# Performance work log

Measured on AMD Instinct MI355X. Metric: run time of the kernel, lower is better.

## Reference

```python
import jax, jax.numpy as jnp
import numpy as np

B, N, C = 32, 197, 768   # batch, tokens (num_patches+1), emb_dim
KW = 197                 # kw_dim = seq_len
L = 12                   # num_layers (weights shared, norms per-layer)
HID = 3072               # mlp hidden = 4*emb_dim


def layer_norm(x, g, b, eps=1e-5):
    mu = jnp.mean(x, axis=-1, keepdims=True)
    var = jnp.var(x, axis=-1, keepdims=True)
    return (x - mu) * jax.lax.rsqrt(var + eps) * g + b


def attention(x, qkv_w, fc_w, fc_b, ln_g, ln_b, fc2_w, fc2_b, num_heads):
    b, n, c = x.shape
    d = c // num_heads
    qkv = (x @ qkv_w).reshape(b, n, 3, num_heads, d)
    q = qkv[:, :, 0].transpose(0, 2, 1, 3)  # [B,H,N,d]
    k = qkv[:, :, 1].transpose(0, 2, 1, 3)
    v = qkv[:, :, 2].transpose(0, 2, 1, 3)
    scale = d ** -0.5
    attn = jnp.einsum('bhnd,bhmd->bhnm', q, k) * scale      # [B,H,N,N]
    attn = attn @ fc_w + fc_b                                # [B,H,N,KW]
    attn = layer_norm(attn, ln_g, ln_b)
    attn = jax.nn.softmax(attn, axis=-1)
    attn = attn.transpose(0, 1, 3, 2)                        # [B,H,KW,N]
    y = jnp.einsum('bhkn,bhnd->bhkd', attn, v)               # [B,H,KW,d]
    # fc2 applied along KW axis of y.transpose(-2,-1): out[b,h,n,d]
    out = jnp.einsum('bhkd,kn->bnhd', y, fc2_w) + fc2_b[None, :, None, None]
    return out.reshape(b, n, c)


def mlp(x, w1, b1, w2, b2):
    return jax.nn.gelu(x @ w1 + b1, approximate=False) @ w2 + b2


def setup_inputs() -> dict:
    key = jax.random.key(0)
    ks = jax.random.split(key, 16)
    s = 0.02
    return {
        'x': jax.random.normal(ks[0], (B, N, C), jnp.float32),
        'qkv_w': jax.random.normal(ks[1], (C, 3 * C), jnp.float32) * s,
        'fc_w': jax.random.normal(ks[2], (N, KW), jnp.float32) * s,
        'fc_b': jnp.zeros((KW,), jnp.float32),
        'attn_ln_g': jnp.ones((KW,), jnp.float32),
        'attn_ln_b': jnp.zeros((KW,), jnp.float32),
        'fc2_w': jax.random.normal(ks[3], (KW, N), jnp.float32) * s,
        'fc2_b': jnp.zeros((N,), jnp.float32),
        'mlp_w1': jax.random.normal(ks[4], (C, HID), jnp.float32) * s,
        'mlp_b1': jnp.zeros((HID,), jnp.float32),
        'mlp_w2': jax.random.normal(ks[5], (HID, C), jnp.float32) * s,
        'mlp_b2': jnp.zeros((C,), jnp.float32),
        'f_ln_g': jnp.ones((L, C), jnp.float32),
        'f_ln_b': jnp.zeros((L, C), jnp.float32),
        'g_ln_g': jnp.ones((L, C), jnp.float32),
        'g_ln_b': jnp.zeros((L, C), jnp.float32),
        'num_heads': 12,
    }


def reference(x, qkv_w, fc_w, fc_b, attn_ln_g, attn_ln_b, fc2_w, fc2_b,
              mlp_w1, mlp_b1, mlp_w2, mlp_b2, f_ln_g, f_ln_b, g_ln_g, g_ln_b,
              num_heads):
    # x -> cat([x,x]) -> reversible stack -> mean of the two halves
    x1, x2 = x, x
    n_layers = f_ln_g.shape[0]
    for i in range(n_layers):
        # y1 = x1 + f(x2); y2 = x2 + g(y1)  (PreNorm wraps f and g)
        y1 = x1 + attention(layer_norm(x2, f_ln_g[i], f_ln_b[i]),
                            qkv_w, fc_w, fc_b, attn_ln_g, attn_ln_b,
                            fc2_w, fc2_b, num_heads)
        y2 = x2 + mlp(layer_norm(y1, g_ln_g[i], g_ln_b[i]),
                      mlp_w1, mlp_b1, mlp_w2, mlp_b2)
        x1, x2 = y1, y2
    return (x1 + x2) * 0.5
```

## Files before the change

kernel.cpp:

```cpp
#include <hip/hip_runtime.h>
#include <math.h>

#define BB   32
#define NN   197
#define CC   768
#define HH   12
#define DD   64
#define KWW  197
#define HIDD 3072
#define NL   12
#define RR   (BB*NN)
#define BHH  (BB*HH)
#define NP   224

typedef __attribute__((ext_vector_type(8))) short short8;
typedef __attribute__((ext_vector_type(4))) float floatx4;
typedef __attribute__((ext_vector_type(4))) unsigned short us4;

__device__ __forceinline__ unsigned short f2bf(float f) {
    unsigned int u = __float_as_uint(f);
    u += 0x7fff + ((u >> 16) & 1);
    return (unsigned short)(u >> 16);
}

__global__ void ln768_kernel(const float* __restrict__ in, const float* __restrict__ g,
                             const float* __restrict__ be, unsigned short* __restrict__ out) {
    int row = blockIdx.x;
    const float* x = in + (size_t)row * CC;
    unsigned short* o = out + (size_t)row * CC;
    int t = threadIdx.x;
    float v0 = x[t], v1 = x[t+256], v2 = x[t+512];
    float s = v0+v1+v2;
    float q = v0*v0+v1*v1+v2*v2;
    for (int off = 1; off < 64; off <<= 1) {
        s += __shfl_xor(s, off, 64);
        q += __shfl_xor(q, off, 64);
    }
    __shared__ float sh[8];
    int wv = t >> 6, ln = t & 63;
    if (ln == 0) { sh[wv] = s; sh[4+wv] = q; }
    __syncthreads();
    s = sh[0]+sh[1]+sh[2]+sh[3];
    q = sh[4]+sh[5]+sh[6]+sh[7];
    float mu  = s * (1.0f/CC);
    float var = q * (1.0f/CC) - mu*mu;
    float rs  = rsqrtf(var + 1e-5f);
    o[t]     = f2bf((v0-mu)*rs*g[t]     + be[t]);
    o[t+256] = f2bf((v1-mu)*rs*g[t+256] + be[t+256]);
    o[t+512] = f2bf((v2-mu)*rs*g[t+512] + be[t+512]);
}

__global__ void init_ln(const float* __restrict__ x, float* __restrict__ x1,
                        float* __restrict__ x2,
                        const float* __restrict__ g, const float* __restrict__ be,
                        unsigned short* __restrict__ out) {
    int row = blockIdx.x;
    const float* xp = x + (size_t)row * CC;
    int t = threadIdx.x;
    float v0 = xp[t], v1 = xp[t+256], v2 = xp[t+512];
    float* a = x1 + (size_t)row * CC;
    float* b = x2 + (size_t)row * CC;
    a[t] = v0; a[t+256] = v1; a[t+512] = v2;
    b[t] = v0; b[t+256] = v1; b[t+512] = v2;
    float s = v0+v1+v2;
    float q = v0*v0+v1*v1+v2*v2;
    for (int off = 1; off < 64; off <<= 1) {
        s += __shfl_xor(s, off, 64);
        q += __shfl_xor(q, off, 64);
    }
    __shared__ float sh[8];
    int wv = t >> 6, ln = t & 63;
    if (ln == 0) { sh[wv] = s; sh[4+wv] = q; }
    __syncthreads();
    s = sh[0]+sh[1]+sh[2]+sh[3];
    q = sh[4]+sh[5]+sh[6]+sh[7];
    float mu  = s * (1.0f/CC);
    float var = q * (1.0f/CC) - mu*mu;
    float rs  = rsqrtf(var + 1e-5f);
    unsigned short* o = out + (size_t)row * CC;
    o[t]     = f2bf((v0-mu)*rs*g[t]     + be[t]);
    o[t+256] = f2bf((v1-mu)*rs*g[t+256] + be[t+256]);
    o[t+512] = f2bf((v2-mu)*rs*g[t+512] + be[t+512]);
}

__global__ void reduce_ln(float* __restrict__ x2, const float* __restrict__ part,
                          const float* __restrict__ b2,
                          const float* __restrict__ g, const float* __restrict__ be,
                          unsigned short* __restrict__ out,
                          const float* __restrict__ x1f, float* __restrict__ outf,
                          int mode) {
    int row = blockIdx.x;
    float* xp = x2 + (size_t)row * CC;
    const float* p0 = part + (size_t)row * CC;
    const float* p1 = part + (size_t)RR*CC + (size_t)row * CC;
    int t = threadIdx.x;
    float v0 = xp[t]     + p0[t]     + p1[t]     + b2[t];
    float v1 = xp[t+256] + p0[t+256] + p1[t+256] + b2[t+256];
    float v2 = xp[t+512] + p0[t+512] + p1[t+512] + b2[t+512];
    xp[t] = v0; xp[t+256] = v1; xp[t+512] = v2;
    if (mode == 2) {
        const float* xo = x1f + (size_t)row * CC;
        float* o = outf + (size_t)row * CC;
        o[t]     = 0.5f*(xo[t]     + v0);
        o[t+256] = 0.5f*(xo[t+256] + v1);
        o[t+512] = 0.5f*(xo[t+512] + v2);
        return;
    }
    float s = v0+v1+v2;
    float q = v0*v0+v1*v1+v2*v2;
    for (int off = 1; off < 64; off <<= 1) {
        s += __shfl_xor(s, off, 64);
        q += __shfl_xor(q, off, 64);
    }
    __shared__ float sh[8];
    int wv = t >> 6, ln = t & 63;
    if (ln == 0) { sh[wv] = s; sh[4+wv] = q; }
    __syncthreads();
    s = sh[0]+sh[1]+sh[2]+sh[3];
    q = sh[4]+sh[5]+sh[6]+sh[7];
    float mu  = s * (1.0f/CC);
    float var = q * (1.0f/CC) - mu*mu;
    float rs  = rsqrtf(var + 1e-5f);
    unsigned short* o = out + (size_t)row * CC;
    o[t]     = f2bf((v0-mu)*rs*g[t]     + be[t]);
    o[t+256] = f2bf((v1-mu)*rs*g[t+256] + be[t+256]);
    o[t+512] = f2bf((v2-mu)*rs*g[t+512] + be[t+512]);
}

__global__ void transpose_cast(const float* __restrict__ in, unsigned short* __restrict__ out,
                               int K, int Nd, int Kpad) {
    __shared__ float tile[32][33];
    int n0 = blockIdx.x*32, k0 = blockIdx.y*32;
    int tx = threadIdx.x & 31, ty = threadIdx.x >> 5;
    #pragma unroll
    for (int i = 0; i < 4; i++) {
        int k = k0 + ty + i*8;
        tile[ty + i*8][tx] = (k < K && n0+tx < Nd) ? in[(size_t)k*Nd + n0 + tx] : 0.f;
    }
    __syncthreads();
    #pragma unroll
    for (int i = 0; i < 4; i++) {
        int n = n0 + ty + i*8;
        if (n < Nd && k0 + tx < Kpad) out[(size_t)n*Kpad + k0 + tx] = f2bf(tile[tx][ty + i*8]);
    }
}

template<int EPI, int KS>
__global__ __launch_bounds__(256) void gemm128(
    const unsigned short* __restrict__ A, const unsigned short* __restrict__ Bt,
    const float* __restrict__ bias, float* __restrict__ Cf, unsigned short* __restrict__ Cb,
    int M, int Nd, int K)
{
    __shared__ unsigned short As[2*128*64];
    __shared__ unsigned short Bs[2*128*64];
    int tid  = threadIdx.x;
    int wv   = tid >> 6, lane = tid & 63;
    int wm   = wv >> 1, wn = wv & 1;
    int quad = lane >> 4, mrow = lane & 15;
    int rl   = lane >> 3, ps = lane & 7;

    int gx   = gridDim.x;
    int nwg  = gx * gridDim.y;
    int orig = blockIdx.y * gx + blockIdx.x;
    int qq = nwg >> 3, rr = nwg & 7;
    int xcd = orig & 7, idx = orig >> 3;
    int wg  = (xcd < rr ? xcd*(qq+1) : rr*(qq+1) + (xcd-rr)*qq) + idx;
    int bm  = (wg / gx) * 128;
    int bn  = (wg % gx) * 128;

    const int Kc    = K / KS;
    const int kbase = (KS > 1) ? blockIdx.z * Kc : 0;
    const int nt    = Kc / 64;

    floatx4 acc[4][4];
    #pragma unroll
    for (int i = 0; i < 4; i++)
        #pragma unroll
        for (int j = 0; j < 4; j++) acc[i][j] = (floatx4){0.f,0.f,0.f,0.f};

#define G128_STAGE(buf, kcol)                                                     \
    do {                                                                          \
        _Pragma("unroll")                                                         \
        for (int i_ = 0; i_ < 4; i_++) {                                          \
            int r_ = wv*32 + i_*8 + rl;                                           \
            int sl_ = ps ^ (r_ & 7);                                              \
            int gr_ = bm + r_; if (gr_ > M-1) gr_ = M-1;                          \
            __builtin_amdgcn_global_load_lds(                                     \
                (const __attribute__((address_space(1))) void*)(A + (size_t)gr_*K + (kcol) + sl_*8), \
                (__attribute__((address_space(3))) void*)(As + (buf)*8192 + (wv*32 + i_*8)*64), \
                16, 0, 0);                                                        \
        }                                                                         \
        _Pragma("unroll")                                                         \
        for (int i_ = 0; i_ < 4; i_++) {                                          \
            int r_ = wv*32 + i_*8 + rl;                                           \
            int sl_ = ps ^ (r_ & 7);                                              \
            int gr_ = bn + r_;                                                    \
            __builtin_amdgcn_global_load_lds(                                     \
                (const __attribute__((address_space(1))) void*)(Bt + (size_t)gr_*K + (kcol) + sl_*8), \
                (__attribute__((address_space(3))) void*)(Bs + (buf)*8192 + (wv*32 + i_*8)*64), \
                16, 0, 0);                                                        \
        }                                                                         \
    } while (0)

    G128_STAGE(0, kbase);
    __syncthreads();

    for (int t = 0; t < nt; ++t) {
        const int c = t & 1;
        if (t + 1 < nt) G128_STAGE(c ^ 1, kbase + (t+1)*64);
        const int cb = c * 8192;
        #pragma unroll
        for (int kk = 0; kk < 2; kk++) {
            short8 af[4], bf[4];
            #pragma unroll
            for (int mi = 0; mi < 4; mi++) {
                int lr = wm*64 + mi*16 + mrow;
                af[mi] = *(const short8*)&As[cb + lr*64 + (((kk<<2)|quad) ^ (lr & 7))*8];
            }
            #pragma unroll
            for (int ni = 0; ni < 4; ni++) {
                int lr = wn*64 + ni*16 + mrow;
                bf[ni] = *(const short8*)&Bs[cb + lr*64 + (((kk<<2)|quad) ^ (lr & 7))*8];
            }
            #pragma unroll
            for (int mi = 0; mi < 4; mi++)
                #pragma unroll
                for (int ni = 0; ni < 4; ni++)
                    acc[mi][ni] = __builtin_amdgcn_mfma_f32_16x16x32_bf16(
                        af[mi], bf[ni], acc[mi][ni], 0, 0, 0);
        }
        __syncthreads();
    }
#undef G128_STAGE

    float* Cfz = (EPI == 5) ? (Cf + (size_t)blockIdx.z * M * Nd) : Cf;
    #pragma unroll
    for (int mi = 0; mi < 4; mi++) {
        int row0 = bm + wm*64 + mi*16 + quad*4;
        #pragma unroll
        for (int ni = 0; ni < 4; ni++) {
            int col = bn + wn*64 + ni*16 + mrow;
            float bv = (EPI == 2) ? bias[col] : 0.f;
            #pragma unroll
            for (int r = 0; r < 4; r++) {
                int row = row0 + r;
                if (row >= M) continue;
                float v = acc[mi][ni][r] + bv;
                if (EPI == 2) {
                    v = v / (1.0f + __expf(-1.5957691216f*v*(1.0f + 0.044715f*v*v)));
                    Cb[(size_t)row*Nd + col] = f2bf(v);
                } else if (EPI == 5) {
                    Cfz[(size_t)row*Nd + col] = v;
                } else if (EPI == 4) {
                    int sel = col / CC;
                    int rem = col - sel*CC;
                    int h = rem >> 6, d = rem & 63;
                    int b = row / NN, n = row - b*NN;
                    int bh = b*HH + h;
                    unsigned short val = f2bf(v);
                    if (sel < 2)
                        Cb[((size_t)sel*BHH + bh)*NN*DD + (size_t)n*DD + d] = val;
                    else
                        Cb[(size_t)2*BHH*NN*DD + (size_t)bh*DD*NP + (size_t)d*NP + n] = val;
                }
            }
        }
    }
}

__global__ __launch_bounds__(256) void attn_score(
    const unsigned short* __restrict__ qb,
    const unsigned short* __restrict__ kb,
    const unsigned short* __restrict__ fw,
    const float* __restrict__ fbias,
    const float* __restrict__ g, const float* __restrict__ be,
    unsigned short* __restrict__ PT)
{
    int bh = blockIdx.y;
    int bm = blockIdx.x * 64;
    __shared__ unsigned short Ks[224*DD];
    __shared__ unsigned short S1s[64*NP];
    __shared__ unsigned short Bs[224*32];
    __shared__ float gls[NP], bls[NP], bbs[NP];
    int tid = threadIdx.x;
    if (tid < NP) {
        bool vc = tid < KWW;
        gls[tid] = vc ? g[tid]     : 1.f;
        bls[tid] = vc ? be[tid]    : 0.f;
        bbs[tid] = vc ? fbias[tid] : 0.f;
    }
    int wv = tid >> 6, lane = tid & 63;
    int quad = lane >> 4, mrow = lane & 15;

    {
        int lrow = lane >> 3, lko = (lane & 7) * 8;
        #pragma unroll
        for (int i = 0; i < 7; i++) {
            int r = wv*56 + i*8 + lrow;
            __builtin_amdgcn_global_load_lds(
                (const __attribute__((address_space(1))) void*)(kb + ((size_t)bh*NN + r)*DD + lko),
                (__attribute__((address_space(3))) void*)(Ks + (size_t)(wv*56 + i*8)*DD),
                16, 0, 0);
        }
    }
    int qrow = bm + wv*16 + mrow; if (qrow > NN-1) qrow = NN-1;
    short8 aq0 = *(const short8*)&qb[((size_t)bh*NN + qrow)*DD + quad*8];
    short8 aq1 = *(const short8*)&qb[((size_t)bh*NN + qrow)*DD + 32 + quad*8];
    __syncthreads();

    #pragma unroll
    for (int ni = 0; ni < 14; ni++) {
        floatx4 a = (floatx4){0.f,0.f,0.f,0.f};
        short8 bf0 = *(const short8*)&Ks[(size_t)(ni*16 + mrow)*DD + quad*8];
        short8 bf1 = *(const short8*)&Ks[(size_t)(ni*16 + mrow)*DD + 32 + quad*8];
        a = __builtin_amdgcn_mfma_f32_16x16x32_bf16(aq0, bf0, a, 0, 0, 0);
        a = __builtin_amdgcn_mfma_f32_16x16x32_bf16(aq1, bf1, a, 0, 0, 0);
        #pragma unroll
        for (int r = 0; r < 4; r++)
            S1s[(size_t)(wv*16 + quad*4 + r)*NP + ni*16 + mrow] = f2bf(a[r]*0.125f);
    }
    __syncthreads();

    floatx4 acc[14];
    #pragma unroll
    for (int j = 0; j < 14; j++) acc[j] = (floatx4){0.f,0.f,0.f,0.f};
    for (int k0 = 0; k0 < 7; k0++) {
        for (int c = wv; c < 14; c += 4) {
            int gr = c*16 + (lane >> 2); if (gr > KWW-1) gr = KWW-1;
            __builtin_amdgcn_global_load_lds(
                (const __attribute__((address_space(1))) void*)(fw + (size_t)gr*NP + k0*32 + (lane & 3)*8),
                (__attribute__((address_space(3))) void*)(Bs + (size_t)(c*16)*32),
                16, 0, 0);
        }
        __syncthreads();
        short8 af = *(const short8*)&S1s[(size_t)(wv*16 + mrow)*NP + k0*32 + quad*8];
        #pragma unroll
        for (int ni = 0; ni < 14; ni++) {
            short8 bf = *(const short8*)&Bs[(size_t)(ni*16 + mrow)*32 + quad*8];
            acc[ni] = __builtin_amdgcn_mfma_f32_16x16x32_bf16(af, bf, acc[ni], 0, 0, 0);
        }
        __syncthreads();
    }

    float s[4] = {}, q[4] = {};
    #pragma unroll
    for (int ni = 0; ni < 14; ni++) {
        int col = ni*16 + mrow;
        float cm = (col < KWW) ? 1.f : 0.f;
        #pragma unroll
        for (int r = 0; r < 4; r++) {
            float x = acc[ni][r] + bbs[col];
            acc[ni][r] = x;
            s[r] += x*cm; q[r] += x*x*cm;
        }
    }
    #pragma unroll
    for (int o = 1; o < 16; o <<= 1)
        #pragma unroll
        for (int r = 0; r < 4; r++) {
            s[r] += __shfl_xor(s[r], o, 64);
            q[r] += __shfl_xor(q[r], o, 64);
        }
    float mu[4], rs[4], mx[4];
    #pragma unroll
    for (int r = 0; r < 4; r++) {
        mu[r] = s[r] * (1.0f/KWW);
        float var = q[r] * (1.0f/KWW) - mu[r]*mu[r];
        rs[r] = rsqrtf(var + 1e-5f);
        mx[r] = -1e30f;
    }
    #pragma unroll
    for (int ni = 0; ni < 14; ni++) {
        int col = ni*16 + mrow;
        bool vc = col < KWW;
        #pragma unroll
        for (int r = 0; r < 4; r++) {
            float x = (acc[ni][r] - mu[r]) * rs[r] * gls[col] + bls[col];
            acc[ni][r] = x;
            if (vc) mx[r] = fmaxf(mx[r], x);
        }
    }
    #pragma unroll
    for (int o = 1; o < 16; o <<= 1)
        #pragma unroll
        for (int r = 0; r < 4; r++)
            mx[r] = fmaxf(mx[r], __shfl_xor(mx[r], o, 64));
    float se[4] = {};
    #pragma unroll
    for (int ni = 0; ni < 14; ni++) {
        int col = ni*16 + mrow;
        float cm = (col < KWW) ? 1.f : 0.f;
        #pragma unroll
        for (int r = 0; r < 4; r++) {
            float p = __expf(acc[ni][r] - mx[r]) * cm;
            acc[ni][r] = p;
            se[r] += p;
        }
    }
    #pragma unroll
    for (int o = 1; o < 16; o <<= 1)
        #pragma unroll
        for (int r = 0; r < 4; r++)
            se[r] += __shfl_xor(se[r], o, 64);
    unsigned short* Pb = PT + (size_t)bh*NP*NP;
    int row0 = bm + wv*16 + quad*4;
    float inv0 = 1.0f/se[0], inv1 = 1.0f/se[1], inv2 = 1.0f/se[2], inv3 = 1.0f/se[3];
    #pragma unroll
    for (int ni = 0; ni < 14; ni++) {
        int col = ni*16 + mrow;
        if (col >= KWW) continue;
        if (row0 + 3 < NN) {
            us4 o = { f2bf(acc[ni][0]*inv0), f2bf(acc[ni][1]*inv1),
                      f2bf(acc[ni][2]*inv2), f2bf(acc[ni][3]*inv3) };
            *(us4*)&Pb[(size_t)col*NP + row0] = o;
        } else {
            float invs[4] = {inv0, inv1, inv2, inv3};
            #pragma unroll
            for (int r = 0; r < 4; r++)
                if (row0 + r < NN)
                    Pb[(size_t)col*NP + row0 + r] = f2bf(acc[ni][r]*invs[r]);
        }
    }
}

__global__ __launch_bounds__(256) void attn_out2(
    const unsigned short* __restrict__ PT,
    const unsigned short* __restrict__ vT,
    const unsigned short* __restrict__ fw,
    const float* __restrict__ bias,
    float* __restrict__ x1)
{
    int dt = blockIdx.x;
    int bh = blockIdx.y; int b = bh / HH, h = bh - b*HH;
    __shared__ unsigned short yT[16*232];
    int wv = threadIdx.x >> 6, lane = threadIdx.x & 63;
    int quad = lane >> 4, mrow = lane & 15;
    const unsigned short* Pb = PT + (size_t)bh*NP*NP;
    const unsigned short* Vb = vT + (size_t)bh*DD*NP + (size_t)(dt*16)*NP;

    short8 bfv[7];
    #pragma unroll
    for (int kc = 0; kc < 7; kc++)
        bfv[kc] = *(const short8*)&Vb[(size_t)mrow*NP + kc*32 + quad*8];
    #pragma unroll
    for (int i = 0; i < 2; i++) {
        int t0 = wv + i*8, t1 = t0 + 4;
        bool v1 = t1 < 14;
        floatx4 a0 = (floatx4){0.f,0.f,0.f,0.f};
        floatx4 a1 = (floatx4){0.f,0.f,0.f,0.f};
        #pragma unroll
        for (int kc = 0; kc < 7; kc++) {
            short8 p0 = *(const short8*)&Pb[(size_t)(t0*16 + mrow)*NP + kc*32 + quad*8];
            a0 = __builtin_amdgcn_mfma_f32_16x16x32_bf16(p0, bfv[kc], a0, 0, 0, 0);
            if (v1) {
                short8 p1 = *(const short8*)&Pb[(size_t)(t1*16 + mrow)*NP + kc*32 + quad*8];
                a1 = __builtin_amdgcn_mfma_f32_16x16x32_bf16(p1, bfv[kc], a1, 0, 0, 0);
            }
        }
        us4 o0 = { f2bf(a0[0]), f2bf(a0[1]), f2bf(a0[2]), f2bf(a0[3]) };
        *(us4*)&yT[mrow*232 + t0*16 + quad*4] = o0;
        if (v1) {
            us4 o1 = { f2bf(a1[0]), f2bf(a1[1]), f2bf(a1[2]), f2bf(a1[3]) };
            *(us4*)&yT[mrow*232 + t1*16 + quad*4] = o1;
        }
    }
    __syncthreads();

    short8 yf[7];
    #pragma unroll
    for (int kc = 0; kc < 7; kc++)
        yf[kc] = *(const short8*)&yT[mrow*232 + kc*32 + quad*8];
    float* xb = x1 + (size_t)b*NN*CC + (size_t)h*DD + dt*16 + mrow;
    #pragma unroll
    for (int i = 0; i < 2; i++) {
        int n0t = wv + i*8, n1t = n0t + 4;
        bool v1 = n1t < 13;
        floatx4 a0 = (floatx4){0.f,0.f,0.f,0.f};
        floatx4 a1 = (floatx4){0.f,0.f,0.f,0.f};
        #pragma unroll
        for (int kc = 0; kc < 7; kc++) {
            short8 f0 = *(const short8*)&fw[(size_t)(n0t*16 + mrow)*NP + kc*32 + quad*8];
            a0 = __builtin_amdgcn_mfma_f32_16x16x32_bf16(f0, yf[kc], a0, 0, 0, 0);
            if (v1) {
                short8 f1 = *(const short8*)&fw[(size_t)(n1t*16 + mrow)*NP + kc*32 + quad*8];
                a1 = __builtin_amdgcn_mfma_f32_16x16x32_bf16(f1, yf[kc], a1, 0, 0, 0);
            }
        }
        #pragma unroll
        for (int r = 0; r < 4; r++) {
            int n = n0t*16 + quad*4 + r;
            if (n < NN) xb[(size_t)n*CC] += a0[r] + bias[n];
        }
        if (v1) {
            #pragma unroll
            for (int r = 0; r < 4; r++) {
                int n = n1t*16 + quad*4 + r;
                if (n < NN) xb[(size_t)n*CC] += a1[r] + bias[n];
            }
        }
    }
}

extern "C" void kernel_launch(void* const* d_in, const int* in_sizes, int n_in,
                              void* d_out, int out_size, void* d_ws, size_t ws_size,
                              hipStream_t stream) {
    const float* x     = (const float*)d_in[0];
    const float* qkv_w = (const float*)d_in[1];
    const float* fc_w  = (const float*)d_in[2];
    const float* fc_b  = (const float*)d_in[3];
    const float* alng  = (const float*)d_in[4];
    const float* alnb  = (const float*)d_in[5];
    const float* fc2w  = (const float*)d_in[6];
    const float* fc2b  = (const float*)d_in[7];
    const float* w1    = (const float*)d_in[8];
    const float* b1    = (const float*)d_in[9];
    const float* w2    = (const float*)d_in[10];
    const float* b2    = (const float*)d_in[11];
    const float* flng  = (const float*)d_in[12];
    const float* flnb  = (const float*)d_in[13];
    const float* glng  = (const float*)d_in[14];
    const float* glnb  = (const float*)d_in[15];
    float* out = (float*)d_out;

    float* ws = (float*)d_ws;
    size_t off = 0;
    float* x1 = ws + off; off += (size_t)RR*CC;
    float* x2 = ws + off; off += (size_t)RR*CC;
    float* part = ws + off; off += (size_t)2*RR*CC;
    unsigned short* lnb = (unsigned short*)(ws + off); off += (size_t)RR*CC/2;
    unsigned short* qkvo = (unsigned short*)(ws + off);
    unsigned short* qb = qkvo;
    unsigned short* kb = qkvo + (size_t)BHH*NN*DD;
    unsigned short* vT = qkvo + (size_t)2*BHH*NN*DD;
    off += ((size_t)2*BHH*NN*DD + (size_t)BHH*DD*NP + 1) / 2;
    unsigned short* PT   = (unsigned short*)(ws + off); off += (size_t)BHH*NP*NP/2;
    unsigned short* hid  = (unsigned short*)(ws + off); off += (size_t)RR*HIDD/2;
    unsigned short* qkv_wt = (unsigned short*)(ws + off); off += (size_t)3*CC*CC/2;
    unsigned short* w1t    = (unsigned short*)(ws + off); off += (size_t)CC*HIDD/2;
    unsigned short* w2t    = (unsigned short*)(ws + off); off += (size_t)CC*HIDD/2;
    unsigned short* fc_wt  = (unsigned short*)(ws + off); off += (size_t)NN*NP/2 + 16;
    unsigned short* fc2_wt = (unsigned short*)(ws + off); off += (size_t)NP*NP/2 + 16;

    hipMemsetAsync(vT, 0, (size_t)BHH*DD*NP*2, stream);
    hipMemsetAsync(fc2_wt, 0, (size_t)NP*NP*2, stream);

    transpose_cast<<<dim3(72, 24), 256, 0, stream>>>(qkv_w, qkv_wt, CC, 3*CC, CC);
    transpose_cast<<<dim3(96, 24), 256, 0, stream>>>(w1, w1t, CC, HIDD, CC);
    transpose_cast<<<dim3(24, 96), 256, 0, stream>>>(w2, w2t, HIDD, CC, HIDD);
    transpose_cast<<<dim3(7, 7),   256, 0, stream>>>(fc_w,  fc_wt,  NN, KWW, NP);
    transpose_cast<<<dim3(7, 7),   256, 0, stream>>>(fc2w,  fc2_wt, KWW, NN, NP);

    init_ln<<<RR, 256, 0, stream>>>(x, x1, x2, flng, flnb, lnb);

    const int MT = (RR + 127) / 128;
    for (int l = 0; l < NL; l++) {
        gemm128<4,1><<<dim3(3*CC/128, MT), 256, 0, stream>>>(
            lnb, qkv_wt, nullptr, nullptr, qb, RR, 3*CC, CC);
        attn_score<<<dim3(4, BHH), 256, 0, stream>>>(
            qb, kb, fc_wt, fc_b, alng, alnb, PT);
        attn_out2<<<dim3(4, BHH), 256, 0, stream>>>(PT, vT, fc2_wt, fc2b, x1);
        ln768_kernel<<<RR, 256, 0, stream>>>(x1, glng + l*CC, glnb + l*CC, lnb);
        gemm128<2,1><<<dim3(HIDD/128, MT), 256, 0, stream>>>(
            lnb, w1t, b1, nullptr, hid, RR, HIDD, CC);
        gemm128<5,2><<<dim3(CC/128, MT, 2), 256, 0, stream>>>(
            hid, w2t, nullptr, part, nullptr, RR, CC, HIDD);
        if (l + 1 < NL) {
            reduce_ln<<<RR, 256, 0, stream>>>(
                x2, part, b2, flng + (l+1)*CC, flnb + (l+1)*CC, lnb,
                nullptr, nullptr, 1);
        } else {
            reduce_ln<<<RR, 256, 0, stream>>>(
                x2, part, b2, nullptr, nullptr, nullptr, x1, out, 2);
        }
    }
}
```

Before: 3.624 ms.

## Single-buffer GEMM LDS tiles and read fc weights directly from global in attn_score

The main GEMM drops its double-buffered LDS prefetch and now loads each K tile, syncs, and computes, which halves its shared memory and may allow more resident blocks, at the cost of losing load/compute overlap. In attn_score the fc weight tile is no longer staged through LDS with two barriers per K step. Each lane now reads its B fragments straight from global memory, and the A fragments are preloaded into registers. The S1 row stride is padded to 232 to reduce bank conflicts, and the fc weight buffer is zero-padded to 224 rows so the direct reads stay in bounds.

```diff
diff --git a/kernel.cpp b/kernel.cpp
--- a/kernel.cpp
+++ b/kernel.cpp
@@ -12,6 +12,7 @@
 #define RR   (BB*NN)
 #define BHH  (BB*HH)
 #define NP   224
+#define SLS  232
 
 typedef __attribute__((ext_vector_type(8))) short short8;
 typedef __attribute__((ext_vector_type(4))) float floatx4;
@@ -151,8 +152,8 @@
     const float* __restrict__ bias, float* __restrict__ Cf, unsigned short* __restrict__ Cb,
     int M, int Nd, int K)
 {
-    __shared__ unsigned short As[2*128*64];
-    __shared__ unsigned short Bs[2*128*64];
+    __shared__ unsigned short As[128*64];
+    __shared__ unsigned short Bs[128*64];
     int tid  = threadIdx.x;
     int wv   = tid >> 6, lane = tid & 63;
     int wm   = wv >> 1, wn = wv & 1;
@@ -170,7 +171,6 @@
 
     const int Kc    = K / KS;
     const int kbase = (KS > 1) ? blockIdx.z * Kc : 0;
-    const int nt    = Kc / 64;
 
     floatx4 acc[4][4];
     #pragma unroll
@@ -178,49 +178,40 @@
         #pragma unroll
         for (int j = 0; j < 4; j++) acc[i][j] = (floatx4){0.f,0.f,0.f,0.f};
 
-#define G128_STAGE(buf, kcol)                                                     \
-    do {                                                                          \
-        _Pragma("unroll")                                                         \
-        for (int i_ = 0; i_ < 4; i_++) {                                          \
-            int r_ = wv*32 + i_*8 + rl;                                           \
-            int sl_ = ps ^ (r_ & 7);                                              \
-            int gr_ = bm + r_; if (gr_ > M-1) gr_ = M-1;                          \
-            __builtin_amdgcn_global_load_lds(                                     \
-                (const __attribute__((address_space(1))) void*)(A + (size_t)gr_*K + (kcol) + sl_*8), \
-                (__attribute__((address_space(3))) void*)(As + (buf)*8192 + (wv*32 + i_*8)*64), \
-                16, 0, 0);                                                        \
-        }                                                                         \
-        _Pragma("unroll")                                                         \
-        for (int i_ = 0; i_ < 4; i_++) {                                          \
-            int r_ = wv*32 + i_*8 + rl;                                           \
-            int sl_ = ps ^ (r_ & 7);                                              \
-            int gr_ = bn + r_;                                                    \
-            __builtin_amdgcn_global_load_lds(                                     \
-                (const __attribute__((address_space(1))) void*)(Bt + (size_t)gr_*K + (kcol) + sl_*8), \
-                (__attribute__((address_space(3))) void*)(Bs + (buf)*8192 + (wv*32 + i_*8)*64), \
-                16, 0, 0);                                                        \
-        }                                                                         \
-    } while (0)
-
-    G128_STAGE(0, kbase);
-    __syncthreads();
-
-    for (int t = 0; t < nt; ++t) {
-        const int c = t & 1;
-        if (t + 1 < nt) G128_STAGE(c ^ 1, kbase + (t+1)*64);
-        const int cb = c * 8192;
+    for (int k0 = kbase; k0 < kbase + Kc; k0 += 64) {
+        #pragma unroll
+        for (int i = 0; i < 4; i++) {
+            int r_ = wv*32 + i*8 + rl;
+            int sl = ps ^ (r_ & 7);
+            int gr = bm + r_; if (gr > M-1) gr = M-1;
+            __builtin_amdgcn_global_load_lds(
+                (const __attribute__((address_space(1))) void*)(A + (size_t)gr*K + k0 + sl*8),
+                (__attribute__((address_space(3))) void*)(As + (wv*32 + i*8)*64),
+                16, 0, 0);
+        }
+        #pragma unroll
+        for (int i = 0; i < 4; i++) {
+            int r_ = wv*32 + i*8 + rl;
+            int sl = ps ^ (r_ & 7);
+            int gr = bn + r_;
+            __builtin_amdgcn_global_load_lds(
+                (const __attribute__((address_space(1))) void*)(Bt + (size_t)gr*K + k0 + sl*8),
+                (__attribute__((address_space(3))) void*)(Bs + (wv*32 + i*8)*64),
+                16, 0, 0);
+        }
+        __syncthreads();
         #pragma unroll
         for (int kk = 0; kk < 2; kk++) {
             short8 af[4], bf[4];
             #pragma unroll
             for (int mi = 0; mi < 4; mi++) {
                 int lr = wm*64 + mi*16 + mrow;
-                af[mi] = *(const short8*)&As[cb + lr*64 + (((kk<<2)|quad) ^ (lr & 7))*8];
+                af[mi] = *(const short8*)&As[lr*64 + (((kk<<2)|quad) ^ (lr & 7))*8];
             }
             #pragma unroll
             for (int ni = 0; ni < 4; ni++) {
                 int lr = wn*64 + ni*16 + mrow;
-                bf[ni] = *(const short8*)&Bs[cb + lr*64 + (((kk<<2)|quad) ^ (lr & 7))*8];
+                bf[ni] = *(const short8*)&Bs[lr*64 + (((kk<<2)|quad) ^ (lr & 7))*8];
             }
             #pragma unroll
             for (int mi = 0; mi < 4; mi++)
@@ -231,7 +222,6 @@
         }
         __syncthreads();
     }
-#undef G128_STAGE
 
     float* Cfz = (EPI == 5) ? (Cf + (size_t)blockIdx.z * M * Nd) : Cf;
     #pragma unroll
@@ -279,8 +269,7 @@
     int bh = blockIdx.y;
     int bm = blockIdx.x * 64;
     __shared__ unsigned short Ks[224*DD];
-    __shared__ unsigned short S1s[64*NP];
-    __shared__ unsigned short Bs[224*32];
+    __shared__ unsigned short S1s[64*SLS];
     __shared__ float gls[NP], bls[NP], bbs[NP];
     int tid = threadIdx.x;
     if (tid < NP) {
@@ -317,29 +306,24 @@
         a = __builtin_amdgcn_mfma_f32_16x16x32_bf16(aq1, bf1, a, 0, 0, 0);
         #pragma unroll
         for (int r = 0; r < 4; r++)
-            S1s[(size_t)(wv*16 + quad*4 + r)*NP + ni*16 + mrow] = f2bf(a[r]*0.125f);
+            S1s[(size_t)(wv*16 + quad*4 + r)*SLS + ni*16 + mrow] = f2bf(a[r]*0.125f);
     }
     __syncthreads();
 
     floatx4 acc[14];
     #pragma unroll
     for (int j = 0; j < 14; j++) acc[j] = (floatx4){0.f,0.f,0.f,0.f};
+    short8 afv[7];
+    #pragma unroll
+    for (int k0 = 0; k0 < 7; k0++)
+        afv[k0] = *(const short8*)&S1s[(size_t)(wv*16 + mrow)*SLS + k0*32 + quad*8];
+    #pragma unroll
     for (int k0 = 0; k0 < 7; k0++) {
-        for (int c = wv; c < 14; c += 4) {
-            int gr = c*16 + (lane >> 2); if (gr > KWW-1) gr = KWW-1;
-            __builtin_amdgcn_global_load_lds(
-                (const __attribute__((address_space(1))) void*)(fw + (size_t)gr*NP + k0*32 + (lane & 3)*8),
-                (__attribute__((address_space(3))) void*)(Bs + (size_t)(c*16)*32),
-                16, 0, 0);
-        }
-        __syncthreads();
-        short8 af = *(const short8*)&S1s[(size_t)(wv*16 + mrow)*NP + k0*32 + quad*8];
         #pragma unroll
         for (int ni = 0; ni < 14; ni++) {
-            short8 bf = *(const short8*)&Bs[(size_t)(ni*16 + mrow)*32 + quad*8];
-            acc[ni] = __builtin_amdgcn_mfma_f32_16x16x32_bf16(af, bf, acc[ni], 0, 0, 0);
-        }
-        __syncthreads();
+            short8 bf = *(const short8*)&fw[(size_t)(ni*16 + mrow)*NP + k0*32 + quad*8];
+            acc[ni] = __builtin_amdgcn_mfma_f32_16x16x32_bf16(afv[k0], bf, acc[ni], 0, 0, 0);
+        }
     }
 
     float s[4] = {}, q[4] = {};
@@ -538,10 +522,11 @@
     unsigned short* qkv_wt = (unsigned short*)(ws + off); off += (size_t)3*CC*CC/2;
     unsigned short* w1t    = (unsigned short*)(ws + off); off += (size_t)CC*HIDD/2;
     unsigned short* w2t    = (unsigned short*)(ws + off); off += (size_t)CC*HIDD/2;
-    unsigned short* fc_wt  = (unsigned short*)(ws + off); off += (size_t)NN*NP/2 + 16;
+    unsigned short* fc_wt  = (unsigned short*)(ws + off); off += (size_t)NP*NP/2 + 16;
     unsigned short* fc2_wt = (unsigned short*)(ws + off); off += (size_t)NP*NP/2 + 16;
 
     hipMemsetAsync(vT, 0, (size_t)BHH*DD*NP*2, stream);
+    hipMemsetAsync(fc_wt, 0, (size_t)NP*NP*2, stream);
     hipMemsetAsync(fc2_wt, 0, (size_t)NP*NP*2, stream);
 
     transpose_cast<<<dim3(72, 24), 256, 0, stream>>>(qkv_w, qkv_wt, CC, 3*CC, CC);
```

New measurement: 3.619 ms. About the same (-0.2%).
